# Optimization experiments

Measured on AMD Instinct MI355X. Metric: run time of the kernel, lower is better.

The kernel has to match this reference:

```python
import jax, jax.numpy as jnp
import numpy as np

D_MODEL = 1024
NUM_HEADS = 16
HEAD_DIM = D_MODEL // NUM_HEADS
ALPHA = 1.0


def setup_inputs() -> dict:
    key = jax.random.key(0)
    ks = jax.random.split(key, 9)
    B, T, D = 2, 2048, D_MODEL
    s = 1.0 / np.sqrt(D)
    inp = {
        "x": jax.random.normal(ks[0], (B, T, D), dtype=jnp.float32),
        "Wq": jax.random.uniform(ks[1], (D, D), jnp.float32, -s, s),
        "bq": jax.random.uniform(ks[2], (D,), jnp.float32, -s, s),
        "Wk": jax.random.uniform(ks[3], (D, D), jnp.float32, -s, s),
        "bk": jax.random.uniform(ks[4], (D,), jnp.float32, -s, s),
        "Wv": jax.random.uniform(ks[5], (D, D), jnp.float32, -s, s),
        "bv": jax.random.uniform(ks[6], (D,), jnp.float32, -s, s),
        "Wo": jax.random.uniform(ks[7], (D, D), jnp.float32, -s, s),
        "bo": jax.random.uniform(ks[8], (D,), jnp.float32, -s, s),
    }
    return inp


def reference(x, Wq, bq, Wk, bk, Wv, bv, Wo, bo):
    B, T, D = x.shape
    H, hd = NUM_HEADS, HEAD_DIM

    def split_heads(y):  # [B,T,D] -> [B,H,T,hd]
        return y.reshape(B, T, H, hd).transpose(0, 2, 1, 3)

    Q = split_heads(x @ Wq.T + bq)
    K = split_heads(x @ Wk.T + bk)
    V = split_heads(x @ Wv.T + bv)

    scores = jnp.einsum('bhid,bhjd->bhij', Q, K) / jnp.sqrt(jnp.float32(hd))

    t = jnp.arange(T)
    delta = t[:, None] - t[None, :]  # [T,T], i - j
    causal_mask = delta < 0          # j > i (strict upper triangle)
    # similarity_power_law decay bias: -(delta)^alpha for delta >= 0, else 0
    decay = jnp.where(causal_mask, 0.0, -(delta.astype(jnp.float32) ** ALPHA))

    scores = jnp.where(causal_mask, -jnp.inf, scores) + decay
    attn = jax.nn.softmax(scores, axis=-1)

    out = jnp.einsum('bhij,bhjd->bhid', attn, V)
    out = out.transpose(0, 2, 1, 3).reshape(B, T, D)
    return out @ Wo.T + bo
```

## Files before the change

### kernel.cpp

```cpp
#include <hip/hip_runtime.h>

#define TT 2048
#define DD 1024
#define HH 16
#define HD 64

typedef __bf16 bf16x8 __attribute__((ext_vector_type(8)));
typedef short short4v __attribute__((ext_vector_type(4)));
typedef float f32x4 __attribute__((ext_vector_type(4)));
typedef unsigned short ushort8v __attribute__((ext_vector_type(8)));

__device__ __forceinline__ unsigned short f2bf(float f) {
  unsigned u = __float_as_uint(f);
  u += 0x7fffu + ((u >> 16) & 1u);
  return (unsigned short)(u >> 16);
}

#if __has_builtin(__builtin_amdgcn_mfma_f32_16x16x16bf16_1k)
__device__ __forceinline__ f32x4 mfma16(short4v a, short4v b, f32x4 c) {
  return __builtin_amdgcn_mfma_f32_16x16x16bf16_1k(a, b, c, 0, 0, 0);
}
#else
__device__ __forceinline__ f32x4 mfma16(short4v a, short4v b, f32x4 c) {
  asm("v_mfma_f32_16x16x16_bf16 %0, %1, %2, %0\n\ts_nop 7\n\ts_nop 7"
      : "+v"(c) : "v"(a), "v"(b));
  return c;
}
#endif

typedef void __attribute__((address_space(1))) as1_void;
typedef void __attribute__((address_space(3))) as3_void;
__device__ __forceinline__ void gl_lds16(const void* g, void* l) {
  __builtin_amdgcn_global_load_lds((as1_void*)g, (as3_void*)l, 16, 0, 0);
}

__global__ __launch_bounds__(256)
void wcmha_cast_all(const float4* __restrict__ x,  const float4* __restrict__ wq,
                    const float4* __restrict__ wk, const float4* __restrict__ wv,
                    const float4* __restrict__ wo,
                    ushort8v* __restrict__ xb,  ushort8v* __restrict__ wqb,
                    ushort8v* __restrict__ wkb, ushort8v* __restrict__ wvb,
                    ushort8v* __restrict__ wob) {
  const int i = blockIdx.x * 256 + threadIdx.x;
  const float4* src;
  ushort8v* dst;
  int off;
  if (i < 524288) {
    src = x; dst = xb; off = i;
  } else {
    int j = i - 524288;
    int sel = j >> 17;
    off = j & 131071;
    const float4* ws_[4] = {wq, wk, wv, wo};
    ushort8v* wd_[4] = {wqb, wkb, wvb, wob};
    src = ws_[sel]; dst = wd_[sel];
  }
  float4 a = src[off * 2];
  float4 b = src[off * 2 + 1];
  ushort8v o;
  o[0] = f2bf(a.x); o[1] = f2bf(a.y); o[2] = f2bf(a.z); o[3] = f2bf(a.w);
  o[4] = f2bf(b.x); o[5] = f2bf(b.y); o[6] = f2bf(b.z); o[7] = f2bf(b.w);
  dst[off] = o;
}

template <int BN_, bool SWAP>
__device__ __forceinline__ void gemm_db(const unsigned short* __restrict__ X,
                                        const unsigned short* __restrict__ W,
                                        int m0, int n0,
                                        unsigned short* As, unsigned short* Bs,
                                        f32x4 acc[4][BN_ / 32]) {
  constexpr int NI = BN_ / 32;
  constexpr int JB = (BN_ * 4) / 256;
  const int tid = threadIdx.x, wid = tid >> 6, lane = tid & 63;
  const int m = lane & 15, quad = lane >> 4;
  const int wm = (wid >> 1) * 64, wn = (wid & 1) * (BN_ / 2);
  const int xq = (quad ^ ((m >> 1) & 3)) * 8;

  const unsigned short* gA[2];
  const unsigned short* gB[JB];
#pragma unroll
  for (int j = 0; j < 2; ++j) {
    int c = wid * 64 + lane + j * 256;
    gA[j] = X + (size_t)(m0 + (c >> 2)) * DD + ((c & 3) ^ ((c >> 3) & 3)) * 8;
  }
#pragma unroll
  for (int j = 0; j < JB; ++j) {
    int c = wid * 64 + lane + j * 256;
    gB[j] = W + (size_t)(n0 + (c >> 2)) * DD + ((c & 3) ^ ((c >> 3) & 3)) * 8;
  }
  unsigned short* lA[2][2];
  unsigned short* lB[2][JB];
#pragma unroll
  for (int p = 0; p < 2; ++p) {
#pragma unroll
    for (int j = 0; j < 2; ++j)
      lA[p][j] = As + p * (128 * 32) + (wid * 64 + j * 256) * 8;
#pragma unroll
    for (int j = 0; j < JB; ++j)
      lB[p][j] = Bs + p * (BN_ * 32) + (wid * 64 + j * 256) * 8;
  }

#pragma unroll
  for (int i = 0; i < 4; ++i)
#pragma unroll
    for (int j = 0; j < NI; ++j) acc[i][j] = (f32x4){0.f, 0.f, 0.f, 0.f};

#pragma unroll
  for (int j = 0; j < 2; ++j) gl_lds16(gA[j], lA[0][j]);
#pragma unroll
  for (int j = 0; j < JB; ++j) gl_lds16(gB[j], lB[0][j]);

  for (int k = 0; k < 32; ++k) {
    const int p = k & 1;
    __syncthreads();
    if (k < 31) {
      const int k1 = (k + 1) * 32;
#pragma unroll
      for (int j = 0; j < 2; ++j) gl_lds16(gA[j] + k1, lA[p ^ 1][j]);
#pragma unroll
      for (int j = 0; j < JB; ++j) gl_lds16(gB[j] + k1, lB[p ^ 1][j]);
    }
    const unsigned short* ap = As + p * (128 * 32);
    const unsigned short* bp = Bs + p * (BN_ * 32);
    bf16x8 af[4], bf[NI];
#pragma unroll
    for (int mi = 0; mi < 4; ++mi)
      af[mi] = *(const bf16x8*)&ap[(wm + mi * 16 + m) * 32 + xq];
#pragma unroll
    for (int ni = 0; ni < NI; ++ni)
      bf[ni] = *(const bf16x8*)&bp[(wn + ni * 16 + m) * 32 + xq];
#pragma unroll
    for (int mi = 0; mi < 4; ++mi)
#pragma unroll
      for (int ni = 0; ni < NI; ++ni)
        acc[mi][ni] = SWAP
            ? __builtin_amdgcn_mfma_f32_16x16x32_bf16(bf[ni], af[mi], acc[mi][ni], 0, 0, 0)
            : __builtin_amdgcn_mfma_f32_16x16x32_bf16(af[mi], bf[ni], acc[mi][ni], 0, 0, 0);
  }
}

__global__ __launch_bounds__(512, 2)
void wcmha_qkv8(const unsigned short* __restrict__ X,
                const unsigned short* __restrict__ Wq,
                const unsigned short* __restrict__ Wk,
                const unsigned short* __restrict__ Wv,
                const float* __restrict__ bq, const float* __restrict__ bk,
                const float* __restrict__ bv,
                unsigned short* __restrict__ Qb,
                unsigned short* __restrict__ Kb,
                unsigned short* __restrict__ Vt) {
  __shared__ unsigned short As[2 * 2 * 256 * 32];
  __shared__ unsigned short Bs[2 * 2 * 256 * 32];
  const int tid = threadIdx.x;
  const int lane = tid & 63, wid = tid >> 6;
  const int m = lane & 15, quad = lane >> 4;
  const int wr = wid >> 2, wc = wid & 3;

  const int mt = blockIdx.x & 15, nt = blockIdx.x >> 4;
  const int m0 = mt * 256;
  const int mat = nt >> 2;
  const int n0w = (nt & 3) * 256;
  const unsigned short* W = (mat == 0) ? Wq : ((mat == 1) ? Wk : Wv);

  const int srow = tid >> 2;
  const int schunk = ((tid & 3) ^ ((tid >> 3) & 3)) * 8;
  const unsigned short* gA[2];
  const unsigned short* gB[2];
  gA[0] = X + (size_t)(m0 + srow) * DD + schunk;
  gA[1] = X + (size_t)(m0 + 128 + srow) * DD + schunk;
  gB[0] = W + (size_t)(n0w + srow) * DD + schunk;
  gB[1] = W + (size_t)(n0w + 128 + srow) * DD + schunk;
  const int ldst = tid * 8;

#define STAGE_A(buf, ks, koff)                                            \
  {                                                                       \
    gl_lds16(gA[0] + (koff), &As[((buf) * 2 + (ks)) * 8192 + ldst]);      \
    gl_lds16(gA[1] + (koff), &As[((buf) * 2 + (ks)) * 8192 + 4096 + ldst]); \
  }
#define STAGE_B(buf, ks, koff)                                            \
  {                                                                       \
    gl_lds16(gB[0] + (koff), &Bs[((buf) * 2 + (ks)) * 8192 + ldst]);      \
    gl_lds16(gB[1] + (koff), &Bs[((buf) * 2 + (ks)) * 8192 + 4096 + ldst]); \
  }

  f32x4 acc[8][4];
#pragma unroll
  for (int i = 0; i < 8; ++i)
#pragma unroll
    for (int j = 0; j < 4; ++j) acc[i][j] = (f32x4){0.f, 0.f, 0.f, 0.f};

  STAGE_A(0, 0, 0) STAGE_B(0, 0, 0)
  STAGE_A(0, 1, 32) STAGE_B(0, 1, 32)
  STAGE_A(1, 0, 64) STAGE_B(1, 0, 64)

  const int xq = (quad ^ ((m >> 1) & 3)) * 8;
  const int arow = wr * 128 + m;
  const int brow = wc * 64 + m;

#pragma unroll 1
  for (int kt = 0; kt < 16; ++kt) {
    const int cur = kt & 1, nxt = cur ^ 1;
    const unsigned short* a0 = &As[(cur * 2 + 0) * 8192];
    const unsigned short* b0 = &Bs[(cur * 2 + 0) * 8192];
    const unsigned short* a1 = &As[(cur * 2 + 1) * 8192];
    const unsigned short* b1 = &Bs[(cur * 2 + 1) * 8192];
    const int kA = (kt + 1) * 64, kB2 = (kt + 2) * 64;
    bf16x8 af[4], bf[4];

    if (kt < 15) { asm volatile("s_waitcnt vmcnt(8)" ::: "memory"); }
    else         { asm volatile("s_waitcnt vmcnt(4)" ::: "memory"); }
    __builtin_amdgcn_s_barrier();
    __builtin_amdgcn_sched_barrier(0);
#pragma unroll
    for (int mi = 0; mi < 4; ++mi)
      af[mi] = *(const bf16x8*)&a0[(arow + mi * 16) * 32 + xq];
#pragma unroll
    for (int ni = 0; ni < 4; ++ni)
      bf[ni] = *(const bf16x8*)&b0[(brow + ni * 16) * 32 + xq];
    if (kt < 15) STAGE_A(nxt, 1, kA + 32)
    asm volatile("s_waitcnt lgkmcnt(0)" ::: "memory");
    __builtin_amdgcn_sched_barrier(0);
    __builtin_amdgcn_s_setprio(1);
#pragma unroll
    for (int mi = 0; mi < 4; ++mi)
#pragma unroll
      for (int ni = 0; ni < 4; ++ni)
        acc[mi][ni] = __builtin_amdgcn_mfma_f32_16x16x32_bf16(bf[ni], af[mi], acc[mi][ni], 0, 0, 0);
    __builtin_amdgcn_s_setprio(0);

    __builtin_amdgcn_s_barrier();
    __builtin_amdgcn_sched_barrier(0);
#pragma unroll
    for (int mi = 0; mi < 4; ++mi)
      af[mi] = *(const bf16x8*)&a0[(arow + (mi + 4) * 16) * 32 + xq];
    if (kt < 15) STAGE_B(nxt, 1, kA + 32)
    asm volatile("s_waitcnt lgkmcnt(0)" ::: "memory");
    __builtin_amdgcn_sched_barrier(0);
    __builtin_amdgcn_s_setprio(1);
#pragma unroll
    for (int mi = 0; mi < 4; ++mi)
#pragma unroll
      for (int ni = 0; ni < 4; ++ni)
        acc[mi + 4][ni] = __builtin_amdgcn_mfma_f32_16x16x32_bf16(bf[ni], af[mi], acc[mi + 4][ni], 0, 0, 0);
    __builtin_amdgcn_s_setprio(0);

    if (kt < 15) { asm volatile("s_waitcnt vmcnt(8)" ::: "memory"); }
    else         { asm volatile("s_waitcnt vmcnt(0)" ::: "memory"); }
    __builtin_amdgcn_s_barrier();
    __builtin_amdgcn_sched_barrier(0);
#pragma unroll
    for (int mi = 0; mi < 4; ++mi)
      af[mi] = *(const bf16x8*)&a1[(arow + mi * 16) * 32 + xq];
#pragma unroll
    for (int ni = 0; ni < 4; ++ni)
      bf[ni] = *(const bf16x8*)&b1[(brow + ni * 16) * 32 + xq];
    if (kt < 14) STAGE_A(cur, 0, kB2)
    asm volatile("s_waitcnt lgkmcnt(0)" ::: "memory");
    __builtin_amdgcn_sched_barrier(0);
    __builtin_amdgcn_s_setprio(1);
#pragma unroll
    for (int mi = 0; mi < 4; ++mi)
#pragma unroll
      for (int ni = 0; ni < 4; ++ni)
        acc[mi][ni] = __builtin_amdgcn_mfma_f32_16x16x32_bf16(bf[ni], af[mi], acc[mi][ni], 0, 0, 0);
    __builtin_amdgcn_s_setprio(0);

    __builtin_amdgcn_s_barrier();
    __builtin_amdgcn_sched_barrier(0);
#pragma unroll
    for (int mi = 0; mi < 4; ++mi)
      af[mi] = *(const bf16x8*)&a1[(arow + (mi + 4) * 16) * 32 + xq];
    if (kt < 14) STAGE_B(cur, 0, kB2)
    asm volatile("s_waitcnt lgkmcnt(0)" ::: "memory");
    __builtin_amdgcn_sched_barrier(0);
    __builtin_amdgcn_s_setprio(1);
#pragma unroll
    for (int mi = 0; mi < 4; ++mi)
#pragma unroll
      for (int ni = 0; ni < 4; ++ni)
        acc[mi + 4][ni] = __builtin_amdgcn_mfma_f32_16x16x32_bf16(bf[ni], af[mi], acc[mi + 4][ni], 0, 0, 0);
    __builtin_amdgcn_s_setprio(0);
  }
#undef STAGE_A
#undef STAGE_B

  if (mat < 2) {
    const float* bias = mat ? bk : bq;
    unsigned short* dst = mat ? Kb : Qb;
#pragma unroll
    for (int mi = 0; mi < 8; ++mi) {
      int row = m0 + wr * 128 + mi * 16 + m;
      int b = row >> 11, t = row & (TT - 1);
#pragma unroll
      for (int ni = 0; ni < 4; ++ni) {
        int col0 = n0w + wc * 64 + ni * 16 + quad * 4;
        int h = col0 >> 6, d0 = col0 & 63;
        float4 bb = *(const float4*)&bias[col0];
        short4v v;
        v[0] = (short)f2bf(acc[mi][ni][0] + bb.x);
        v[1] = (short)f2bf(acc[mi][ni][1] + bb.y);
        v[2] = (short)f2bf(acc[mi][ni][2] + bb.z);
        v[3] = (short)f2bf(acc[mi][ni][3] + bb.w);
        *(short4v*)&dst[((size_t)(b * HH + h) * TT + t) * HD + d0] = v;
      }
    }
  } else {
#pragma unroll
    for (int mi = 0; mi < 8; ++mi) {
      int row = m0 + wr * 128 + mi * 16 + m;
      int b = row >> 11, t = row & (TT - 1);
#pragma unroll
      for (int ni = 0; ni < 4; ++ni) {
        int col0 = n0w + wc * 64 + ni * 16 + quad * 4;
        int h = col0 >> 6, d0 = col0 & 63;
#pragma unroll
        for (int r = 0; r < 4; ++r) {
          float bb = bv[col0 + r];
          Vt[((size_t)(b * HH + h) * HD + d0 + r) * TT + t] =
              f2bf(acc[mi][ni][r] + bb);
        }
      }
    }
  }
}

__global__ __launch_bounds__(256)
void wcmha_gemm_out(const unsigned short* __restrict__ X,
                    const unsigned short* __restrict__ W,
                    const float* __restrict__ bias,
                    float* __restrict__ Y) {
  __shared__ unsigned short As[2 * 128 * 32];
  __shared__ unsigned short Bs[2 * 64 * 32];
  const int m0 = blockIdx.x * 128;
  const int n0 = blockIdx.y * 64;
  const int lane = threadIdx.x & 63, wid = threadIdx.x >> 6;
  const int m = lane & 15, quad = lane >> 4;
  const int wm = (wid >> 1) * 64, wn = (wid & 1) * 32;

  f32x4 acc[4][2];
  gemm_db<64, true>(X, W, m0, n0, As, Bs, acc);

#pragma unroll
  for (int mi = 0; mi < 4; ++mi) {
    int row = m0 + wm + mi * 16 + m;
#pragma unroll
    for (int ni = 0; ni < 2; ++ni) {
      int col0 = n0 + wn + ni * 16 + quad * 4;
      float4 bb = *(const float4*)&bias[col0];
      float4 o;
      o.x = acc[mi][ni][0] + bb.x;
      o.y = acc[mi][ni][1] + bb.y;
      o.z = acc[mi][ni][2] + bb.z;
      o.w = acc[mi][ni][3] + bb.w;
      *(float4*)&Y[(size_t)row * DD + col0] = o;
    }
  }
}

__global__ __launch_bounds__(256)
void wcmha_attn(const unsigned short* __restrict__ Qb,
                const unsigned short* __restrict__ Kb,
                const unsigned short* __restrict__ Vt,
                unsigned short* __restrict__ O) {
  const int wid = threadIdx.x >> 6, lane = threadIdx.x & 63;
  const int gw = (blockIdx.x << 2) + wid;
  const int qt = gw & 127, bh = gw >> 7;
  const int qbase = qt << 4;
  const int il = lane & 15, quad = lane >> 4;
  const int ig = qbase + il;

  const unsigned short* q_ptr = Qb + (size_t)bh * TT * HD;
  const unsigned short* k_ptr = Kb + (size_t)bh * TT * HD;
  const unsigned short* v_ptr = Vt + (size_t)bh * HD * TT;

  const bf16x8 qf0 = *(const bf16x8*)(q_ptr + (size_t)ig * HD + quad * 8);
  const bf16x8 qf1 = *(const bf16x8*)(q_ptr + (size_t)ig * HD + 32 + quad * 8);

  const int j0 = (qbase >= 48) ? qbase - 48 : 0;

  f32x4 st[4];
#pragma unroll
  for (int jt = 0; jt < 4; ++jt) {
    const unsigned short* kp = k_ptr + (size_t)(j0 + jt * 16 + il) * HD;
    bf16x8 k0 = *(const bf16x8*)(kp + quad * 8);
    bf16x8 k1 = *(const bf16x8*)(kp + 32 + quad * 8);
    f32x4 a = {0.f, 0.f, 0.f, 0.f};
    a = __builtin_amdgcn_mfma_f32_16x16x32_bf16(k0, qf0, a, 0, 0, 0);
    a = __builtin_amdgcn_mfma_f32_16x16x32_bf16(k1, qf1, a, 0, 0, 0);
    st[jt] = a;
  }

  float mloc = -3.0e38f;
#pragma unroll
  for (int jt = 0; jt < 4; ++jt)
#pragma unroll
    for (int r = 0; r < 4; ++r) {
      int jg = j0 + jt * 16 + quad * 4 + r;
      float v = (jg > ig) ? -3.0e38f : st[jt][r] * 0.125f - (float)(ig - jg);
      st[jt][r] = v;
      mloc = fmaxf(mloc, v);
    }
  mloc = fmaxf(mloc, __shfl_xor(mloc, 16));
  mloc = fmaxf(mloc, __shfl_xor(mloc, 32));

  float rs = 0.f;
  short4v pf[4];
#pragma unroll
  for (int jt = 0; jt < 4; ++jt)
#pragma unroll
    for (int r = 0; r < 4; ++r) {
      float p = __expf(st[jt][r] - mloc);
      rs += p;
      pf[jt][r] = (short)f2bf(p);
    }
  rs += __shfl_xor(rs, 16);
  rs += __shfl_xor(rs, 32);

  f32x4 o_acc[4];
#pragma unroll
  for (int nt = 0; nt < 4; ++nt) o_acc[nt] = (f32x4){0.f, 0.f, 0.f, 0.f};
#pragma unroll
  for (int jt = 0; jt < 4; ++jt)
#pragma unroll
    for (int nt = 0; nt < 4; ++nt) {
      short4v vf = *(const short4v*)(v_ptr + (size_t)(nt * 16 + il) * TT +
                                     j0 + jt * 16 + quad * 4);
      o_acc[nt] = mfma16(vf, pf[jt], o_acc[nt]);
    }

  const float inv_l = 1.f / rs;
  const int b = bh >> 4, hh = bh & 15;
  unsigned short* ob = O + ((size_t)(b * TT + ig)) * DD + hh * HD;
#pragma unroll
  for (int nt = 0; nt < 4; ++nt) {
    short4v v;
#pragma unroll
    for (int r = 0; r < 4; ++r) v[r] = (short)f2bf(o_acc[nt][r] * inv_l);
    *(short4v*)&ob[nt * 16 + quad * 4] = v;
  }
}

extern "C" void kernel_launch(void* const* d_in, const int* in_sizes, int n_in,
                              void* d_out, int out_size, void* d_ws, size_t ws_size,
                              hipStream_t stream) {
  const float* x  = (const float*)d_in[0];
  const float* Wq = (const float*)d_in[1];
  const float* bq = (const float*)d_in[2];
  const float* Wk = (const float*)d_in[3];
  const float* bk = (const float*)d_in[4];
  const float* Wv = (const float*)d_in[5];
  const float* bv = (const float*)d_in[6];
  const float* Wo = (const float*)d_in[7];
  const float* bo = (const float*)d_in[8];

  char* ws = (char*)d_ws;
  unsigned short* xb  = (unsigned short*)(ws);
  unsigned short* wqb = (unsigned short*)(ws + (8u << 20));
  unsigned short* wkb = wqb + (1u << 20);
  unsigned short* wvb = wkb + (1u << 20);
  unsigned short* wob = wvb + (1u << 20);
  unsigned short* Qb  = (unsigned short*)(ws + (16u << 20));
  unsigned short* Kb  = (unsigned short*)(ws + (24u << 20));
  unsigned short* Vt  = (unsigned short*)(ws + (32u << 20));
  unsigned short* Ob  = xb;

  wcmha_cast_all<<<4096, 256, 0, stream>>>(
      (const float4*)x, (const float4*)Wq, (const float4*)Wk,
      (const float4*)Wv, (const float4*)Wo,
      (ushort8v*)xb, (ushort8v*)wqb, (ushort8v*)wkb, (ushort8v*)wvb,
      (ushort8v*)wob);

  wcmha_qkv8<<<192, 512, 0, stream>>>(xb, wqb, wkb, wvb,
                                      bq, bk, bv, Qb, Kb, Vt);

  wcmha_attn<<<1024, 256, 0, stream>>>(Qb, Kb, Vt, Ob);

  wcmha_gemm_out<<<dim3(32, 16), 256, 0, stream>>>(Ob, wob, bo, (float*)d_out);
}
```

Baseline: 163.8 us.

## Retile fused QKV GEMM to 256x192 tiles for a full 256-block grid

```diff
diff --git a/kernel.cpp b/kernel.cpp
--- a/kernel.cpp
+++ b/kernel.cpp
@@ -141,16 +141,14 @@
 
 __global__ __launch_bounds__(512, 2)
 void wcmha_qkv8(const unsigned short* __restrict__ X,
-                const unsigned short* __restrict__ Wq,
-                const unsigned short* __restrict__ Wk,
-                const unsigned short* __restrict__ Wv,
+                const unsigned short* __restrict__ WQKV,
                 const float* __restrict__ bq, const float* __restrict__ bk,
                 const float* __restrict__ bv,
                 unsigned short* __restrict__ Qb,
                 unsigned short* __restrict__ Kb,
                 unsigned short* __restrict__ Vt) {
   __shared__ unsigned short As[2 * 2 * 256 * 32];
-  __shared__ unsigned short Bs[2 * 2 * 256 * 32];
+  __shared__ unsigned short Bs[2 * 2 * 192 * 32];
   const int tid = threadIdx.x;
   const int lane = tid & 63, wid = tid >> 6;
   const int m = lane & 15, quad = lane >> 4;
@@ -158,73 +156,74 @@
 
   const int mt = blockIdx.x & 15, nt = blockIdx.x >> 4;
   const int m0 = mt * 256;
-  const int mat = nt >> 2;
-  const int n0w = (nt & 3) * 256;
-  const unsigned short* W = (mat == 0) ? Wq : ((mat == 1) ? Wk : Wv);
+  const int n0w = nt * 192;
 
   const int srow = tid >> 2;
   const int schunk = ((tid & 3) ^ ((tid >> 3) & 3)) * 8;
-  const unsigned short* gA[2];
-  const unsigned short* gB[2];
-  gA[0] = X + (size_t)(m0 + srow) * DD + schunk;
-  gA[1] = X + (size_t)(m0 + 128 + srow) * DD + schunk;
-  gB[0] = W + (size_t)(n0w + srow) * DD + schunk;
-  gB[1] = W + (size_t)(n0w + 128 + srow) * DD + schunk;
+  const unsigned short* gA0 = X + (size_t)(m0 + srow) * DD + schunk;
+  const unsigned short* gA1 = gA0 + (size_t)128 * DD;
+  const unsigned short* gB0 = WQKV + (size_t)(n0w + srow) * DD + schunk;
+  const unsigned short* gB1 = gB0 + (size_t)128 * DD;
   const int ldst = tid * 8;
 
-#define STAGE_A(buf, ks, koff)                                            \
-  {                                                                       \
-    gl_lds16(gA[0] + (koff), &As[((buf) * 2 + (ks)) * 8192 + ldst]);      \
-    gl_lds16(gA[1] + (koff), &As[((buf) * 2 + (ks)) * 8192 + 4096 + ldst]); \
-  }
-#define STAGE_B(buf, ks, koff)                                            \
-  {                                                                       \
-    gl_lds16(gB[0] + (koff), &Bs[((buf) * 2 + (ks)) * 8192 + ldst]);      \
-    gl_lds16(gB[1] + (koff), &Bs[((buf) * 2 + (ks)) * 8192 + 4096 + ldst]); \
-  }
-
-  f32x4 acc[8][4];
+#define SA(buf, ks, koff)                                                     \
+  {                                                                           \
+    gl_lds16(gA0 + (koff), &As[((buf) * 2 + (ks)) * 8192 + ldst]);            \
+    gl_lds16(gA1 + (koff), &As[((buf) * 2 + (ks)) * 8192 + 4096 + ldst]);     \
+  }
+#define SB(buf, ks, koff)                                                     \
+  {                                                                           \
+    gl_lds16(gB0 + (koff), &Bs[((buf) * 2 + (ks)) * 6144 + ldst]);            \
+    if (tid < 256)                                                            \
+      gl_lds16(gB1 + (koff), &Bs[((buf) * 2 + (ks)) * 6144 + 4096 + ldst]);   \
+  }
+
+  f32x4 acc[8][3];
 #pragma unroll
   for (int i = 0; i < 8; ++i)
 #pragma unroll
-    for (int j = 0; j < 4; ++j) acc[i][j] = (f32x4){0.f, 0.f, 0.f, 0.f};
-
-  STAGE_A(0, 0, 0) STAGE_B(0, 0, 0)
-  STAGE_A(0, 1, 32) STAGE_B(0, 1, 32)
-  STAGE_A(1, 0, 64) STAGE_B(1, 0, 64)
+    for (int j = 0; j < 3; ++j) acc[i][j] = (f32x4){0.f, 0.f, 0.f, 0.f};
+
+  SA(0, 0, 0) SB(0, 0, 0)
+  SA(0, 1, 32) SB(0, 1, 32)
+  SA(1, 0, 64) SB(1, 0, 64)
 
   const int xq = (quad ^ ((m >> 1) & 3)) * 8;
   const int arow = wr * 128 + m;
-  const int brow = wc * 64 + m;
+  const int brow = wc * 48 + m;
 
 #pragma unroll 1
   for (int kt = 0; kt < 16; ++kt) {
     const int cur = kt & 1, nxt = cur ^ 1;
     const unsigned short* a0 = &As[(cur * 2 + 0) * 8192];
-    const unsigned short* b0 = &Bs[(cur * 2 + 0) * 8192];
+    const unsigned short* b0 = &Bs[(cur * 2 + 0) * 6144];
     const unsigned short* a1 = &As[(cur * 2 + 1) * 8192];
-    const unsigned short* b1 = &Bs[(cur * 2 + 1) * 8192];
-    const int kA = (kt + 1) * 64, kB2 = (kt + 2) * 64;
-    bf16x8 af[4], bf[4];
-
-    if (kt < 15) { asm volatile("s_waitcnt vmcnt(8)" ::: "memory"); }
-    else         { asm volatile("s_waitcnt vmcnt(4)" ::: "memory"); }
+    const unsigned short* b1 = &Bs[(cur * 2 + 1) * 6144];
+    const int kA = (kt + 1) * 64 + 32;
+    const int kB2 = (kt + 2) * 64;
+    bf16x8 af[4], bf[3];
+
+    if (kt < 15) {
+      if (wid < 4) { asm volatile("s_waitcnt vmcnt(8)" ::: "memory"); }
+      else         { asm volatile("s_waitcnt vmcnt(6)" ::: "memory"); }
+    } else {
+      if (wid < 4) { asm volatile("s_waitcnt vmcnt(4)" ::: "memory"); }
+      else         { asm volatile("s_waitcnt vmcnt(3)" ::: "memory"); }
+    }
     __builtin_amdgcn_s_barrier();
     __builtin_amdgcn_sched_barrier(0);
 #pragma unroll
     for (int mi = 0; mi < 4; ++mi)
       af[mi] = *(const bf16x8*)&a0[(arow + mi * 16) * 32 + xq];
 #pragma unroll
-    for (int ni = 0; ni < 4; ++ni)
+    for (int ni = 0; ni < 3; ++ni)
       bf[ni] = *(const bf16x8*)&b0[(brow + ni * 16) * 32 + xq];
-    if (kt < 15) STAGE_A(nxt, 1, kA + 32)
-    asm volatile("s_waitcnt lgkmcnt(0)" ::: "memory");
-    __builtin_amdgcn_sched_barrier(0);
+    if (kt < 15) SA(nxt, 1, kA)
     __builtin_amdgcn_s_setprio(1);
 #pragma unroll
     for (int mi = 0; mi < 4; ++mi)
 #pragma unroll
-      for (int ni = 0; ni < 4; ++ni)
+      for (int ni = 0; ni < 3; ++ni)
         acc[mi][ni] = __builtin_amdgcn_mfma_f32_16x16x32_bf16(bf[ni], af[mi], acc[mi][ni], 0, 0, 0);
     __builtin_amdgcn_s_setprio(0);
 
@@ -233,35 +232,35 @@
 #pragma unroll
     for (int mi = 0; mi < 4; ++mi)
       af[mi] = *(const bf16x8*)&a0[(arow + (mi + 4) * 16) * 32 + xq];
-    if (kt < 15) STAGE_B(nxt, 1, kA + 32)
-    asm volatile("s_waitcnt lgkmcnt(0)" ::: "memory");
-    __builtin_amdgcn_sched_barrier(0);
+    if (kt < 15) SB(nxt, 1, kA)
     __builtin_amdgcn_s_setprio(1);
 #pragma unroll
     for (int mi = 0; mi < 4; ++mi)
 #pragma unroll
-      for (int ni = 0; ni < 4; ++ni)
+      for (int ni = 0; ni < 3; ++ni)
         acc[mi + 4][ni] = __builtin_amdgcn_mfma_f32_16x16x32_bf16(bf[ni], af[mi], acc[mi + 4][ni], 0, 0, 0);
     __builtin_amdgcn_s_setprio(0);
 
-    if (kt < 15) { asm volatile("s_waitcnt vmcnt(8)" ::: "memory"); }
-    else         { asm volatile("s_waitcnt vmcnt(0)" ::: "memory"); }
+    if (kt < 15) {
+      if (wid < 4) { asm volatile("s_waitcnt vmcnt(8)" ::: "memory"); }
+      else         { asm volatile("s_waitcnt vmcnt(6)" ::: "memory"); }
+    } else {
+      asm volatile("s_waitcnt vmcnt(0)" ::: "memory");
+    }
     __builtin_amdgcn_s_barrier();
     __builtin_amdgcn_sched_barrier(0);
 #pragma unroll
     for (int mi = 0; mi < 4; ++mi)
       af[mi] = *(const bf16x8*)&a1[(arow + mi * 16) * 32 + xq];
 #pragma unroll
-    for (int ni = 0; ni < 4; ++ni)
+    for (int ni = 0; ni < 3; ++ni)
       bf[ni] = *(const bf16x8*)&b1[(brow + ni * 16) * 32 + xq];
-    if (kt < 14) STAGE_A(cur, 0, kB2)
-    asm volatile("s_waitcnt lgkmcnt(0)" ::: "memory");
-    __builtin_amdgcn_sched_barrier(0);
+    if (kt < 14) SA(cur, 0, kB2)
     __builtin_amdgcn_s_setprio(1);
 #pragma unroll
     for (int mi = 0; mi < 4; ++mi)
 #pragma unroll
-      for (int ni = 0; ni < 4; ++ni)
+      for (int ni = 0; ni < 3; ++ni)
         acc[mi][ni] = __builtin_amdgcn_mfma_f32_16x16x32_bf16(bf[ni], af[mi], acc[mi][ni], 0, 0, 0);
     __builtin_amdgcn_s_setprio(0);
 
@@ -270,52 +269,41 @@
 #pragma unroll
     for (int mi = 0; mi < 4; ++mi)
       af[mi] = *(const bf16x8*)&a1[(arow + (mi + 4) * 16) * 32 + xq];
-    if (kt < 14) STAGE_B(cur, 0, kB2)
-    asm volatile("s_waitcnt lgkmcnt(0)" ::: "memory");
-    __builtin_amdgcn_sched_barrier(0);
+    if (kt < 14) SB(cur, 0, kB2)
     __builtin_amdgcn_s_setprio(1);
 #pragma unroll
     for (int mi = 0; mi < 4; ++mi)
 #pragma unroll
-      for (int ni = 0; ni < 4; ++ni)
+      for (int ni = 0; ni < 3; ++ni)
         acc[mi + 4][ni] = __builtin_amdgcn_mfma_f32_16x16x32_bf16(bf[ni], af[mi], acc[mi + 4][ni], 0, 0, 0);
     __builtin_amdgcn_s_setprio(0);
   }
-#undef STAGE_A
-#undef STAGE_B
-
-  if (mat < 2) {
-    const float* bias = mat ? bk : bq;
-    unsigned short* dst = mat ? Kb : Qb;
-#pragma unroll
-    for (int mi = 0; mi < 8; ++mi) {
-      int row = m0 + wr * 128 + mi * 16 + m;
-      int b = row >> 11, t = row & (TT - 1);
-#pragma unroll
-      for (int ni = 0; ni < 4; ++ni) {
-        int col0 = n0w + wc * 64 + ni * 16 + quad * 4;
-        int h = col0 >> 6, d0 = col0 & 63;
-        float4 bb = *(const float4*)&bias[col0];
+#undef SA
+#undef SB
+
+#pragma unroll
+  for (int mi = 0; mi < 8; ++mi) {
+    int row = m0 + wr * 128 + mi * 16 + m;
+    int b = row >> 11, t = row & (TT - 1);
+#pragma unroll
+    for (int ni = 0; ni < 3; ++ni) {
+      int col0 = n0w + wc * 48 + ni * 16 + quad * 4;
+      int mat = col0 >> 10, lc = col0 & 1023;
+      int h = lc >> 6, d0 = lc & 63;
+      if (mat < 2) {
+        const float* bias = mat ? bk : bq;
+        unsigned short* dst = mat ? Kb : Qb;
+        float4 bb = *(const float4*)&bias[lc];
         short4v v;
         v[0] = (short)f2bf(acc[mi][ni][0] + bb.x);
         v[1] = (short)f2bf(acc[mi][ni][1] + bb.y);
         v[2] = (short)f2bf(acc[mi][ni][2] + bb.z);
         v[3] = (short)f2bf(acc[mi][ni][3] + bb.w);
         *(short4v*)&dst[((size_t)(b * HH + h) * TT + t) * HD + d0] = v;
-      }
-    }
-  } else {
-#pragma unroll
-    for (int mi = 0; mi < 8; ++mi) {
-      int row = m0 + wr * 128 + mi * 16 + m;
-      int b = row >> 11, t = row & (TT - 1);
-#pragma unroll
-      for (int ni = 0; ni < 4; ++ni) {
-        int col0 = n0w + wc * 64 + ni * 16 + quad * 4;
-        int h = col0 >> 6, d0 = col0 & 63;
+      } else {
 #pragma unroll
         for (int r = 0; r < 4; ++r) {
-          float bb = bv[col0 + r];
+          float bb = bv[lc + r];
           Vt[((size_t)(b * HH + h) * HD + d0 + r) * TT + t] =
               f2bf(acc[mi][ni][r] + bb);
         }
@@ -470,8 +458,7 @@
       (ushort8v*)xb, (ushort8v*)wqb, (ushort8v*)wkb, (ushort8v*)wvb,
       (ushort8v*)wob);
 
-  wcmha_qkv8<<<192, 512, 0, stream>>>(xb, wqb, wkb, wvb,
-                                      bq, bk, bv, Qb, Kb, Vt);
+  wcmha_qkv8<<<256, 512, 0, stream>>>(xb, wqb, bq, bk, bv, Qb, Kb, Vt);
 
   wcmha_attn<<<1024, 256, 0, stream>>>(Qb, Kb, Vt, Ob);
 
```

Result: no change. 162.2 us (-1.0%).
